# Performance work log

Measured on AMD Instinct MI355X. Metric: run time of the kernel, lower is better.

Reference implementation:

```python
import jax, jax.numpy as jnp
import numpy as np

HIDDEN = 32          # hardcoded in nn.Linear(latent_dim, 32)
THRESHOLD = 1.5      # hardcoded adjacency threshold


def setup_inputs() -> dict:
    key = jax.random.key(0)
    ks = jax.random.split(key, 12)
    N, LATENT, MSG = 8192, 128, 64

    def lin(kw, kb, fan_in, fan_out):
        bound = 1.0 / np.sqrt(fan_in)
        W = jax.random.uniform(kw, (fan_in, fan_out), jnp.float32, -bound, bound)
        b = jax.random.uniform(kb, (fan_out,), jnp.float32, -bound, bound)
        return W, b

    enc_W, enc_b = lin(ks[0], ks[1], LATENT, HIDDEN)
    msg_W, msg_b = lin(ks[2], ks[3], HIDDEN, MSG)
    upd_W, upd_b = lin(ks[4], ks[5], HIDDEN + MSG, HIDDEN)
    out_W, out_b = lin(ks[6], ks[7], HIDDEN, MSG)

    z = jax.random.normal(ks[8], (N, LATENT), jnp.float32)
    agent_dists = jax.random.normal(ks[9], (N, N), jnp.float32)
    tau = jnp.float32(1.0)
    return {
        "z": z, "tau": tau, "agent_dists": agent_dists,
        "enc_W": enc_W, "enc_b": enc_b,
        "msg_W": msg_W, "msg_b": msg_b,
        "upd_W": upd_W, "upd_b": upd_b,
        "out_W": out_W, "out_b": out_b,
    }


def reference(z, tau, agent_dists, enc_W, enc_b, msg_W, msg_b, upd_W, upd_b, out_W, out_b):
    N = agent_dists.shape[0]
    h = jax.nn.relu(z @ enc_W + enc_b)                       # [N, 32]
    # vectorized adjacency: off-diagonal entries with dist < threshold
    idx = jnp.arange(N)
    off_diag = idx[:, None] != idx[None, :]
    adj = jnp.where(off_diag & (agent_dists < THRESHOLD), 1.0, 0.0).astype(z.dtype)  # [N, N]
    messages = h @ msg_W + msg_b                             # [N, MSG]
    aggregated = adj @ messages                              # [N, MSG]
    h2 = jax.nn.relu(jnp.concatenate([h, aggregated], axis=-1) @ upd_W + upd_b)  # [N, 32]
    logits = h2 @ out_W + out_b                              # [N, MSG]
    # gumbel_softmax (soft): softmax((logits + gumbel) / tau)
    gkey = jax.random.key(42)
    u = jax.random.uniform(gkey, logits.shape, logits.dtype, 1e-10, 1.0)
    gumbel = -jnp.log(-jnp.log(u))
    return jax.nn.softmax((logits + gumbel) / tau, axis=-1)
```

## Files before the change

### kernel.cpp

```cpp
#include <hip/hip_runtime.h>
#include <hip/hip_bf16.h>
#include <math.h>

#define N_AGENTS 8192
#define LATENT   128
#define HIDDEN   32
#define MSG      64
#define CONCAT   96
#define THRESH   1.5f
#define KSPLIT   16
#define SLICE    (N_AGENTS / KSPLIT)
#define SGRP     4

typedef float f32x4  __attribute__((ext_vector_type(4)));
typedef short bf16x8 __attribute__((ext_vector_type(8)));

__device__ __forceinline__ unsigned rotl32(unsigned x, unsigned r) {
  return (x << r) | (x >> (32u - r));
}
__device__ __forceinline__ void tf_round(unsigned &x0, unsigned &x1, unsigned r) {
  x0 += x1; x1 = rotl32(x1, r); x1 ^= x0;
}
__device__ __forceinline__ uint2 threefry_0_42(unsigned x0, unsigned x1) {
  const unsigned k0 = 0u, k1 = 42u, k2 = 0x1BD11BDAu ^ 0u ^ 42u;
  x0 += k0; x1 += k1;
  tf_round(x0,x1,13); tf_round(x0,x1,15); tf_round(x0,x1,26); tf_round(x0,x1, 6);
  x0 += k1; x1 += k2 + 1u;
  tf_round(x0,x1,17); tf_round(x0,x1,29); tf_round(x0,x1,16); tf_round(x0,x1,24);
  x0 += k2; x1 += k0 + 2u;
  tf_round(x0,x1,13); tf_round(x0,x1,15); tf_round(x0,x1,26); tf_round(x0,x1, 6);
  x0 += k0; x1 += k1 + 3u;
  tf_round(x0,x1,17); tf_round(x0,x1,29); tf_round(x0,x1,16); tf_round(x0,x1,24);
  x0 += k1; x1 += k2 + 4u;
  tf_round(x0,x1,13); tf_round(x0,x1,15); tf_round(x0,x1,26); tf_round(x0,x1, 6);
  x0 += k2; x1 += k0 + 5u;
  return make_uint2(x0, x1);
}

__device__ __forceinline__ float gumbel_at(unsigned idx) {
  const unsigned H = (N_AGENTS * MSG) / 2;
  unsigned bits;
  if (idx < H) {
    uint2 o = threefry_0_42(idx, idx + H);
    bits = o.x;
  } else {
    uint2 o = threefry_0_42(idx - H, idx);
    bits = o.y;
  }
  float f = __uint_as_float((bits >> 9) | 0x3f800000u) - 1.0f;
  float u = fmaxf(1e-10f, f + 1e-10f);
  return -logf(-logf(u));
}

__device__ __forceinline__ unsigned short f2bf(float x) {
  unsigned u = __float_as_uint(x);
  u += 0x7FFFu + ((u >> 16) & 1u);
  return (unsigned short)(u >> 16);
}

__global__ __launch_bounds__(256) void k_encode(
    const float* __restrict__ z, const float* __restrict__ encW, const float* __restrict__ encB,
    const float* __restrict__ msgW, const float* __restrict__ msgB,
    float* __restrict__ h_out, unsigned* __restrict__ msgR_u32,
    unsigned short* __restrict__ msgT)
{
  __shared__ float z_s[8][LATENT];
  __shared__ float encW_s[LATENT*HIDDEN];
  __shared__ float msgW_s[HIDDEN*MSG];
  __shared__ float h_s[8][HIDDEN];
  __shared__ float m_s[8][MSG];
  const int t  = threadIdx.x;
  const int r0 = blockIdx.x * 8;

  #pragma unroll
  for (int it = 0; it < 16; ++it) encW_s[t + 256*it] = encW[t + 256*it];
  #pragma unroll
  for (int it = 0; it < 8; ++it)  msgW_s[t + 256*it] = msgW[t + 256*it];
  #pragma unroll
  for (int it = 0; it < 4; ++it) {
    int q = t + 256*it;
    z_s[q >> 7][q & 127] = z[(size_t)r0*LATENT + q];
  }
  __syncthreads();

  {
    int r = t >> 5, c = t & 31;
    float acc = encB[c];
    #pragma unroll
    for (int k = 0; k < LATENT; ++k) acc = fmaf(z_s[r][k], encW_s[k*HIDDEN + c], acc);
    float hv = fmaxf(acc, 0.0f);
    h_s[r][c] = hv;
    h_out[(size_t)(r0 + r)*HIDDEN + c] = hv;
  }
  __syncthreads();

  #pragma unroll
  for (int it = 0; it < 2; ++it) {
    int r = (t >> 6) + 4*it, c = t & 63;
    float acc = msgB[c];
    #pragma unroll
    for (int k = 0; k < HIDDEN; ++k) acc = fmaf(h_s[r][k], msgW_s[k*MSG + c], acc);
    m_s[r][c] = acc;
  }
  __syncthreads();

  {
    int r = t >> 5, c0 = (t & 31) * 2;
    unsigned lo = f2bf(m_s[r][c0]), hi = f2bf(m_s[r][c0 + 1]);
    msgR_u32[(size_t)(r0 + r)*32 + (t & 31)] = lo | (hi << 16);
  }
  {
    int c = t & 63, rr = (t >> 6) * 2;
    unsigned lo = f2bf(m_s[rr][c]), hi = f2bf(m_s[rr + 1][c]);
    *(unsigned*)(msgT + (size_t)c*N_AGENTS + r0 + rr) = lo | (hi << 16);
  }
}

__device__ __forceinline__ bf16x8 adj_frag(f32x4 lo, f32x4 hi) {
  union { bf16x8 v; unsigned u[4]; } r;
  r.u[0] = (lo.x < THRESH ? 0x3F80u : 0u) | (lo.y < THRESH ? 0x3F800000u : 0u);
  r.u[1] = (lo.z < THRESH ? 0x3F80u : 0u) | (lo.w < THRESH ? 0x3F800000u : 0u);
  r.u[2] = (hi.x < THRESH ? 0x3F80u : 0u) | (hi.y < THRESH ? 0x3F800000u : 0u);
  r.u[3] = (hi.z < THRESH ? 0x3F80u : 0u) | (hi.w < THRESH ? 0x3F800000u : 0u);
  return r.v;
}

__global__ __launch_bounds__(256, 4) void k_agg(
    const float* __restrict__ dists, const unsigned short* __restrict__ msgT,
    float* __restrict__ P)
{
  __shared__ float red_s[4][32][MSG];
  const int lane = threadIdx.x & 63;
  const int wv   = threadIdx.x >> 6;
  const int rowTile  = blockIdx.x & 255;
  const int sliceGrp = blockIdx.x >> 8;
  const int row0 = rowTile * 32;
  const int k0   = (sliceGrp * 4 + wv) * SLICE;
  const int m = lane & 15, q = lane >> 4;

  const float* a0p = dists + (size_t)(row0 + m) * N_AGENTS + k0 + q*8;
  const float* a1p = a0p + (size_t)16 * N_AGENTS;
  const unsigned short* b0p = msgT + (size_t)(m)      * N_AGENTS + k0 + q*8;
  const unsigned short* b1p = msgT + (size_t)(m + 16) * N_AGENTS + k0 + q*8;
  const unsigned short* b2p = msgT + (size_t)(m + 32) * N_AGENTS + k0 + q*8;
  const unsigned short* b3p = msgT + (size_t)(m + 48) * N_AGENTS + k0 + q*8;

  f32x4 acc[2][4];
  #pragma unroll
  for (int g = 0; g < 2; ++g)
    #pragma unroll
    for (int nt = 0; nt < 4; ++nt) acc[g][nt] = (f32x4)0.0f;

  #pragma unroll
  for (int kk = 0; kk < SLICE / 32; ++kk) {
    const int off = kk * 32;
    f32x4 a00 = __builtin_nontemporal_load((const f32x4*)(a0p + off));
    f32x4 a01 = __builtin_nontemporal_load((const f32x4*)(a0p + off + 4));
    f32x4 a10 = __builtin_nontemporal_load((const f32x4*)(a1p + off));
    f32x4 a11 = __builtin_nontemporal_load((const f32x4*)(a1p + off + 4));
    bf16x8 b0 = *(const bf16x8*)(b0p + off);
    bf16x8 b1 = *(const bf16x8*)(b1p + off);
    bf16x8 b2 = *(const bf16x8*)(b2p + off);
    bf16x8 b3 = *(const bf16x8*)(b3p + off);
    bf16x8 af0 = adj_frag(a00, a01);
    bf16x8 af1 = adj_frag(a10, a11);
    acc[0][0] = __builtin_amdgcn_mfma_f32_16x16x32_bf16(af0, b0, acc[0][0], 0, 0, 0);
    acc[0][1] = __builtin_amdgcn_mfma_f32_16x16x32_bf16(af0, b1, acc[0][1], 0, 0, 0);
    acc[0][2] = __builtin_amdgcn_mfma_f32_16x16x32_bf16(af0, b2, acc[0][2], 0, 0, 0);
    acc[0][3] = __builtin_amdgcn_mfma_f32_16x16x32_bf16(af0, b3, acc[0][3], 0, 0, 0);
    acc[1][0] = __builtin_amdgcn_mfma_f32_16x16x32_bf16(af1, b0, acc[1][0], 0, 0, 0);
    acc[1][1] = __builtin_amdgcn_mfma_f32_16x16x32_bf16(af1, b1, acc[1][1], 0, 0, 0);
    acc[1][2] = __builtin_amdgcn_mfma_f32_16x16x32_bf16(af1, b2, acc[1][2], 0, 0, 0);
    acc[1][3] = __builtin_amdgcn_mfma_f32_16x16x32_bf16(af1, b3, acc[1][3], 0, 0, 0);
  }

  #pragma unroll
  for (int g = 0; g < 2; ++g)
    #pragma unroll
    for (int nt = 0; nt < 4; ++nt)
      #pragma unroll
      for (int r = 0; r < 4; ++r)
        red_s[wv][g*16 + q*4 + r][nt*16 + m] = acc[g][nt][r];
  __syncthreads();

  const int row = threadIdx.x >> 3;
  const int c0  = (threadIdx.x & 7) * 8;
  f32x4 s0 = *(const f32x4*)&red_s[0][row][c0];
  f32x4 s1 = *(const f32x4*)&red_s[0][row][c0 + 4];
  #pragma unroll
  for (int w2 = 1; w2 < 4; ++w2) {
    s0 += *(const f32x4*)&red_s[w2][row][c0];
    s1 += *(const f32x4*)&red_s[w2][row][c0 + 4];
  }
  float* dst = P + ((size_t)sliceGrp * N_AGENTS + row0 + row) * MSG + c0;
  *(f32x4*)dst       = s0;
  *(f32x4*)(dst + 4) = s1;
}

__global__ __launch_bounds__(256) void k_out(
    const float* __restrict__ P, const float* __restrict__ dists,
    const unsigned short* __restrict__ msgR,
    const float* __restrict__ h_in,
    const float* __restrict__ updW, const float* __restrict__ updB,
    const float* __restrict__ outW, const float* __restrict__ outB,
    const float* __restrict__ tau, float* __restrict__ out)
{
  __shared__ float x_s[4][CONCAT];
  __shared__ float h2_s[4][HIDDEN];
  const int w    = threadIdx.x >> 6;
  const int lane = threadIdx.x & 63;
  const int i    = blockIdx.x * 4 + w;

  float agg = 0.0f;
  #pragma unroll
  for (int g = 0; g < SGRP; ++g)
    agg += P[((size_t)g * N_AGENTS + i) * MSG + lane];

  float dii = dists[(size_t)i * (N_AGENTS + 1)];
  if (dii < THRESH) {
    unsigned short us = msgR[(size_t)i * MSG + lane];
    agg -= __uint_as_float(((unsigned)us) << 16);
  }

  x_s[w][HIDDEN + lane] = agg;
  if (lane < HIDDEN) x_s[w][lane] = h_in[(size_t)i * HIDDEN + lane];
  __syncthreads();

  if (lane < HIDDEN) {
    float acc = updB[lane];
    #pragma unroll
    for (int k = 0; k < CONCAT; ++k) acc = fmaf(x_s[w][k], updW[k*HIDDEN + lane], acc);
    h2_s[w][lane] = fmaxf(acc, 0.0f);
  }
  __syncthreads();

  float lg = outB[lane];
  #pragma unroll
  for (int c = 0; c < HIDDEN; ++c) lg = fmaf(h2_s[w][c], outW[c*MSG + lane], lg);

  float tv = (lg + gumbel_at((unsigned)i*64u + (unsigned)lane)) / tau[0];

  float mx = tv;
  #pragma unroll
  for (int off = 32; off > 0; off >>= 1) mx = fmaxf(mx, __shfl_xor(mx, off, 64));
  float ex = expf(tv - mx);
  float sm = ex;
  #pragma unroll
  for (int off = 32; off > 0; off >>= 1) sm += __shfl_xor(sm, off, 64);
  out[(size_t)i * MSG + lane] = ex / sm;
}

extern "C" void kernel_launch(void* const* d_in, const int* in_sizes, int n_in,
                              void* d_out, int out_size, void* d_ws, size_t ws_size,
                              hipStream_t stream) {
  const float* z     = (const float*)d_in[0];
  const float* tau   = (const float*)d_in[1];
  const float* dists = (const float*)d_in[2];
  const float* encW  = (const float*)d_in[3];
  const float* encB  = (const float*)d_in[4];
  const float* msgW  = (const float*)d_in[5];
  const float* msgB  = (const float*)d_in[6];
  const float* updW  = (const float*)d_in[7];
  const float* updB  = (const float*)d_in[8];
  const float* outW  = (const float*)d_in[9];
  const float* outB  = (const float*)d_in[10];
  (void)in_sizes; (void)n_in; (void)out_size; (void)ws_size;

  char* ws = (char*)d_ws;
  float*          P_ws  = (float*)(ws);
  float*          h_ws  = (float*)(ws + (8u<<20));
  unsigned short* msgR  = (unsigned short*)(ws + (9u<<20));
  unsigned short* msgT  = (unsigned short*)(ws + (10u<<20));
  float* out = (float*)d_out;

  hipLaunchKernelGGL(k_encode, dim3(N_AGENTS/8), dim3(256), 0, stream,
                     z, encW, encB, msgW, msgB, h_ws, (unsigned*)msgR, msgT);
  hipLaunchKernelGGL(k_agg, dim3(256 * SGRP), dim3(256), 0, stream,
                     dists, msgT, P_ws);
  hipLaunchKernelGGL(k_out, dim3(N_AGENTS/4), dim3(256), 0, stream,
                     P_ws, dists, msgR, h_ws, updW, updB, outW, outB, tau, out);
}
```

Before: 430.6 us.

## Stage distance tiles into LDS via direct global-to-LDS loads, drop in-block reduction

The aggregation kernel now copies 32x256 chunks of the distance matrix into padded shared memory using global_load_lds, so each block reads full contiguous row segments before the MFMA loop. Each wave then works on an interleaved k sub-range of every chunk. The per-block cross-wave shared-memory reduction is removed, and each wave writes its own partial, giving 16 partials that the output kernel sums. The aim is more coalesced, streaming DRAM reads of the 256MB matrix. The cost is two barriers per chunk, no double buffering, and four times more partial-sum traffic through the workspace.

```diff
diff --git a/kernel.cpp b/kernel.cpp
--- a/kernel.cpp
+++ b/kernel.cpp
@@ -8,9 +8,8 @@
 #define MSG      64
 #define CONCAT   96
 #define THRESH   1.5f
-#define KSPLIT   16
-#define SLICE    (N_AGENTS / KSPLIT)
-#define SGRP     4
+#define NPART    16
+#define ROWSTRIDE 260
 
 typedef float f32x4  __attribute__((ext_vector_type(4)));
 typedef short bf16x8 __attribute__((ext_vector_type(8)));
@@ -58,6 +57,12 @@
   return (unsigned short)(u >> 16);
 }
 
+__device__ __forceinline__ void stage16(const float* g, float* l) {
+  __builtin_amdgcn_global_load_lds(
+      (const __attribute__((address_space(1))) void*)g,
+      (__attribute__((address_space(3))) void*)l, 16, 0, 0);
+}
+
 __global__ __launch_bounds__(256) void k_encode(
     const float* __restrict__ z, const float* __restrict__ encW, const float* __restrict__ encB,
     const float* __restrict__ msgW, const float* __restrict__ msgB,
@@ -129,72 +134,67 @@
     const float* __restrict__ dists, const unsigned short* __restrict__ msgT,
     float* __restrict__ P)
 {
-  __shared__ float red_s[4][32][MSG];
+  __shared__ __align__(16) float ldsA[32 * ROWSTRIDE];
   const int lane = threadIdx.x & 63;
   const int wv   = threadIdx.x >> 6;
   const int rowTile  = blockIdx.x & 255;
   const int sliceGrp = blockIdx.x >> 8;
   const int row0 = rowTile * 32;
-  const int k0   = (sliceGrp * 4 + wv) * SLICE;
+  const int kblk = sliceGrp * 2048;
   const int m = lane & 15, q = lane >> 4;
 
-  const float* a0p = dists + (size_t)(row0 + m) * N_AGENTS + k0 + q*8;
-  const float* a1p = a0p + (size_t)16 * N_AGENTS;
-  const unsigned short* b0p = msgT + (size_t)(m)      * N_AGENTS + k0 + q*8;
-  const unsigned short* b1p = msgT + (size_t)(m + 16) * N_AGENTS + k0 + q*8;
-  const unsigned short* b2p = msgT + (size_t)(m + 32) * N_AGENTS + k0 + q*8;
-  const unsigned short* b3p = msgT + (size_t)(m + 48) * N_AGENTS + k0 + q*8;
-
   f32x4 acc[2][4];
   #pragma unroll
   for (int g = 0; g < 2; ++g)
     #pragma unroll
     for (int nt = 0; nt < 4; ++nt) acc[g][nt] = (f32x4)0.0f;
 
-  #pragma unroll
-  for (int kk = 0; kk < SLICE / 32; ++kk) {
-    const int off = kk * 32;
-    f32x4 a00 = __builtin_nontemporal_load((const f32x4*)(a0p + off));
-    f32x4 a01 = __builtin_nontemporal_load((const f32x4*)(a0p + off + 4));
-    f32x4 a10 = __builtin_nontemporal_load((const f32x4*)(a1p + off));
-    f32x4 a11 = __builtin_nontemporal_load((const f32x4*)(a1p + off + 4));
-    bf16x8 b0 = *(const bf16x8*)(b0p + off);
-    bf16x8 b1 = *(const bf16x8*)(b1p + off);
-    bf16x8 b2 = *(const bf16x8*)(b2p + off);
-    bf16x8 b3 = *(const bf16x8*)(b3p + off);
-    bf16x8 af0 = adj_frag(a00, a01);
-    bf16x8 af1 = adj_frag(a10, a11);
-    acc[0][0] = __builtin_amdgcn_mfma_f32_16x16x32_bf16(af0, b0, acc[0][0], 0, 0, 0);
-    acc[0][1] = __builtin_amdgcn_mfma_f32_16x16x32_bf16(af0, b1, acc[0][1], 0, 0, 0);
-    acc[0][2] = __builtin_amdgcn_mfma_f32_16x16x32_bf16(af0, b2, acc[0][2], 0, 0, 0);
-    acc[0][3] = __builtin_amdgcn_mfma_f32_16x16x32_bf16(af0, b3, acc[0][3], 0, 0, 0);
-    acc[1][0] = __builtin_amdgcn_mfma_f32_16x16x32_bf16(af1, b0, acc[1][0], 0, 0, 0);
-    acc[1][1] = __builtin_amdgcn_mfma_f32_16x16x32_bf16(af1, b1, acc[1][1], 0, 0, 0);
-    acc[1][2] = __builtin_amdgcn_mfma_f32_16x16x32_bf16(af1, b2, acc[1][2], 0, 0, 0);
-    acc[1][3] = __builtin_amdgcn_mfma_f32_16x16x32_bf16(af1, b3, acc[1][3], 0, 0, 0);
-  }
-
+  const unsigned short* bbase = msgT + (size_t)m * N_AGENTS;
+
+  for (int chunk = 0; chunk < 8; ++chunk) {
+    const int kb = kblk + chunk * 256;
+    #pragma unroll
+    for (int rr = 0; rr < 8; ++rr) {
+      const int r = wv * 8 + rr;
+      stage16(dists + (size_t)(row0 + r) * N_AGENTS + kb + lane * 4,
+              &ldsA[r * ROWSTRIDE]);
+    }
+    __syncthreads();
+
+    #pragma unroll
+    for (int ks = 0; ks < 2; ++ks) {
+      const int kf = wv * 64 + ks * 32 + q * 8;
+      f32x4 a00 = *(const f32x4*)&ldsA[m * ROWSTRIDE + kf];
+      f32x4 a01 = *(const f32x4*)&ldsA[m * ROWSTRIDE + kf + 4];
+      f32x4 a10 = *(const f32x4*)&ldsA[(m + 16) * ROWSTRIDE + kf];
+      f32x4 a11 = *(const f32x4*)&ldsA[(m + 16) * ROWSTRIDE + kf + 4];
+      bf16x8 af0 = adj_frag(a00, a01);
+      bf16x8 af1 = adj_frag(a10, a11);
+      const size_t kg = (size_t)kb + kf;
+      bf16x8 b0 = *(const bf16x8*)(bbase + (size_t)0  * N_AGENTS + kg);
+      bf16x8 b1 = *(const bf16x8*)(bbase + (size_t)16 * N_AGENTS + kg);
+      bf16x8 b2 = *(const bf16x8*)(bbase + (size_t)32 * N_AGENTS + kg);
+      bf16x8 b3 = *(const bf16x8*)(bbase + (size_t)48 * N_AGENTS + kg);
+      acc[0][0] = __builtin_amdgcn_mfma_f32_16x16x32_bf16(af0, b0, acc[0][0], 0, 0, 0);
+      acc[0][1] = __builtin_amdgcn_mfma_f32_16x16x32_bf16(af0, b1, acc[0][1], 0, 0, 0);
+      acc[0][2] = __builtin_amdgcn_mfma_f32_16x16x32_bf16(af0, b2, acc[0][2], 0, 0, 0);
+      acc[0][3] = __builtin_amdgcn_mfma_f32_16x16x32_bf16(af0, b3, acc[0][3], 0, 0, 0);
+      acc[1][0] = __builtin_amdgcn_mfma_f32_16x16x32_bf16(af1, b0, acc[1][0], 0, 0, 0);
+      acc[1][1] = __builtin_amdgcn_mfma_f32_16x16x32_bf16(af1, b1, acc[1][1], 0, 0, 0);
+      acc[1][2] = __builtin_amdgcn_mfma_f32_16x16x32_bf16(af1, b2, acc[1][2], 0, 0, 0);
+      acc[1][3] = __builtin_amdgcn_mfma_f32_16x16x32_bf16(af1, b3, acc[1][3], 0, 0, 0);
+    }
+    __syncthreads();
+  }
+
+  float* dst = P + (size_t)(sliceGrp * 4 + wv) * N_AGENTS * MSG;
   #pragma unroll
   for (int g = 0; g < 2; ++g)
     #pragma unroll
     for (int nt = 0; nt < 4; ++nt)
       #pragma unroll
       for (int r = 0; r < 4; ++r)
-        red_s[wv][g*16 + q*4 + r][nt*16 + m] = acc[g][nt][r];
-  __syncthreads();
-
-  const int row = threadIdx.x >> 3;
-  const int c0  = (threadIdx.x & 7) * 8;
-  f32x4 s0 = *(const f32x4*)&red_s[0][row][c0];
-  f32x4 s1 = *(const f32x4*)&red_s[0][row][c0 + 4];
-  #pragma unroll
-  for (int w2 = 1; w2 < 4; ++w2) {
-    s0 += *(const f32x4*)&red_s[w2][row][c0];
-    s1 += *(const f32x4*)&red_s[w2][row][c0 + 4];
-  }
-  float* dst = P + ((size_t)sliceGrp * N_AGENTS + row0 + row) * MSG + c0;
-  *(f32x4*)dst       = s0;
-  *(f32x4*)(dst + 4) = s1;
+        dst[(size_t)(row0 + g*16 + q*4 + r) * MSG + nt*16 + m] = acc[g][nt][r];
 }
 
 __global__ __launch_bounds__(256) void k_out(
@@ -213,7 +213,7 @@
 
   float agg = 0.0f;
   #pragma unroll
-  for (int g = 0; g < SGRP; ++g)
+  for (int g = 0; g < NPART; ++g)
     agg += P[((size_t)g * N_AGENTS + i) * MSG + lane];
 
   float dii = dists[(size_t)i * (N_AGENTS + 1)];
@@ -268,14 +268,14 @@
 
   char* ws = (char*)d_ws;
   float*          P_ws  = (float*)(ws);
-  float*          h_ws  = (float*)(ws + (8u<<20));
-  unsigned short* msgR  = (unsigned short*)(ws + (9u<<20));
-  unsigned short* msgT  = (unsigned short*)(ws + (10u<<20));
+  float*          h_ws  = (float*)(ws + (32u<<20));
+  unsigned short* msgR  = (unsigned short*)(ws + (33u<<20));
+  unsigned short* msgT  = (unsigned short*)(ws + (34u<<20));
   float* out = (float*)d_out;
 
   hipLaunchKernelGGL(k_encode, dim3(N_AGENTS/8), dim3(256), 0, stream,
                      z, encW, encB, msgW, msgB, h_ws, (unsigned*)msgR, msgT);
-  hipLaunchKernelGGL(k_agg, dim3(256 * SGRP), dim3(256), 0, stream,
+  hipLaunchKernelGGL(k_agg, dim3(256 * 4), dim3(256), 0, stream,
                      dists, msgT, P_ws);
   hipLaunchKernelGGL(k_out, dim3(N_AGENTS/4), dim3(256), 0, stream,
                      P_ws, dists, msgR, h_ws, updW, updB, outW, outB, tau, out);
```

Measured after the change: 420.1 us. -2.4%, faster.
